# Performance work log

Measured on AMD Instinct MI355X. Metric: run time of the kernel, lower is better.

## Reference

```python
import jax, jax.numpy as jnp
import numpy as np

D_MODEL = 1024
NUM_HEADS = 16
HEAD_DIM = D_MODEL // NUM_HEADS


def setup_inputs() -> dict:
    key = jax.random.key(0)
    k1, k2, k3, k4, k5 = jax.random.split(key, 5)
    B, S = 2, 2048
    X = jax.random.normal(k1, (B, S, D_MODEL), dtype=jnp.float32)
    Wqkv = jax.random.normal(k2, (3 * D_MODEL, D_MODEL), dtype=jnp.float32) * 0.02
    bqkv = jax.random.normal(k3, (3 * D_MODEL,), dtype=jnp.float32) * 0.02
    Wo = jax.random.normal(k4, (D_MODEL, D_MODEL), dtype=jnp.float32) * 0.02
    bo = jax.random.normal(k5, (D_MODEL,), dtype=jnp.float32) * 0.02
    return {"X": X, "Wqkv": Wqkv, "bqkv": bqkv, "Wo": Wo, "bo": bo}


def reference(X, Wqkv, bqkv, Wo, bo):
    B, S, D = X.shape
    # fused QKV projection (torch Linear: x @ W.T + b)
    qkv = X @ Wqkv.T + bqkv                                  # [B, S, 3D]
    qkv = qkv.reshape(B, S, NUM_HEADS, 3 * HEAD_DIM)
    qkv = jnp.transpose(qkv, (0, 2, 1, 3))                   # [B, H, S, 3*hd]
    q, k, v = jnp.split(qkv, 3, axis=-1)                     # each [B, H, S, hd]
    # naive scaled dot-product attention (materializes full SxS scores)
    scale = 1.0 / jnp.sqrt(jnp.asarray(HEAD_DIM, dtype=X.dtype))
    scores = jnp.einsum("bhqd,bhkd->bhqk", q, k) * scale     # [B, H, S, S]
    attn = jax.nn.softmax(scores, axis=-1)
    values = jnp.einsum("bhqk,bhkd->bhqd", attn, v)          # [B, H, S, hd]
    values = jnp.transpose(values, (0, 2, 1, 3)).reshape(B, S, D)
    return values @ Wo.T + bo
```

## Files before the change

kernel.cpp:

```cpp
#include <hip/hip_runtime.h>

#define DM    1024
#define NH    16
#define HD    64
#define SEQ   2048
#define BATCH 2
#define NQKV  3072
#define MTOT  4096

using half2v = __attribute__((ext_vector_type(2))) _Float16;
using half4  = __attribute__((ext_vector_type(4))) _Float16;
using half8  = __attribute__((ext_vector_type(8))) _Float16;
using f32x4  = __attribute__((ext_vector_type(4))) float;

typedef const __attribute__((address_space(1))) unsigned int* gp_t;
typedef __attribute__((address_space(3))) unsigned int* lp_t;

__device__ __forceinline__ void gl2lds16(const void* g, void* l) {
    __builtin_amdgcn_global_load_lds((gp_t)g, (lp_t)l, 16, 0, 0);
}

__device__ __forceinline__ f32x4 fzero4() {
    f32x4 v; v[0] = 0.f; v[1] = 0.f; v[2] = 0.f; v[3] = 0.f; return v;
}

__device__ __forceinline__ int sw8(int row, int col) {
    return (row << 6) | ((((col >> 3) ^ row) & 7) << 3) | (col & 7);
}

#define CSCALE 0.18033688011112042f

__device__ __forceinline__ half2v expp2(float a, float b) {
    return __builtin_bit_cast(half2v, __builtin_amdgcn_cvt_pkrtz(
        __builtin_amdgcn_exp2f(a), __builtin_amdgcn_exp2f(b)));
}

#define ACQ(N) do {                                             \
    asm volatile("s_waitcnt vmcnt(" #N ")" ::: "memory");       \
    __builtin_amdgcn_sched_barrier(0);                          \
    __builtin_amdgcn_s_barrier();                               \
    __builtin_amdgcn_sched_barrier(0);                          \
} while (0)
#define REL() do {                                              \
    __builtin_amdgcn_sched_barrier(0);                          \
    asm volatile("s_waitcnt lgkmcnt(0)" ::: "memory");          \
    __builtin_amdgcn_s_barrier();                               \
    __builtin_amdgcn_sched_barrier(0);                          \
} while (0)

__global__ __launch_bounds__(256) void cvt_all(const float* __restrict__ X,
                                               const float* __restrict__ W1,
                                               const float* __restrict__ W2,
                                               const float* __restrict__ bqkv,
                                               float* __restrict__ bscaled,
                                               _Float16* __restrict__ out) {
    const int nX = MTOT * DM / 4, nW1 = NQKV * DM / 4, nW2 = DM * DM / 4;
    int i = blockIdx.x * 256 + threadIdx.x;
    if (i < NQKV) {
        const float b = bqkv[i];
        bscaled[i] = ((i % 192) < 64) ? b * CSCALE : b;
    }
    if (i >= nX + nW1 + nW2) return;
    float4 f;
    float sc = 1.0f;
    if (i < nX) {
        f = reinterpret_cast<const float4*>(X)[i];
    } else if (i < nX + nW1) {
        const int off = i - nX;
        f = reinterpret_cast<const float4*>(W1)[off];
        const int row = off >> 8;
        if ((row % 192) < 64) sc = CSCALE;
    } else {
        f = reinterpret_cast<const float4*>(W2)[i - nX - nW1];
    }
    half4 h;
    h[0] = (_Float16)(f.x * sc); h[1] = (_Float16)(f.y * sc);
    h[2] = (_Float16)(f.z * sc); h[3] = (_Float16)(f.w * sc);
    reinterpret_cast<half4*>(out)[i] = h;
}

template <bool OUT_F16>
__global__ __launch_bounds__(256) void gemm_nt(const _Float16* __restrict__ A,
                                               const _Float16* __restrict__ B,
                                               const float* __restrict__ bias,
                                               void* __restrict__ Cout,
                                               int M, int N, int K) {
    __shared__ _Float16 lA[128 * 64];
    __shared__ _Float16 lB[128 * 64];
    const int tid = threadIdx.x;
    const int m0 = blockIdx.y * 128, n0 = blockIdx.x * 128;
    const int wave = tid >> 6, lane = tid & 63, quad = lane >> 4, l15 = lane & 15;
    const int wm = (wave & 1) * 64, wn = (wave >> 1) * 64;

    f32x4 acc[4][4];
#pragma unroll
    for (int i = 0; i < 4; ++i)
#pragma unroll
        for (int j = 0; j < 4; ++j) acc[i][j] = fzero4();

    const int cperm = (((tid & 7) ^ (tid >> 3)) & 7) * 8;
    const _Float16* Ab = A + (long)(m0 + (tid >> 3)) * K + cperm;
    const _Float16* Bb = B + (long)(n0 + (tid >> 3)) * K + cperm;
    char* lAp = (char*)lA + tid * 16;
    char* lBp = (char*)lB + tid * 16;

    for (int kt = 0; kt < K; kt += 64) {
        __syncthreads();
#pragma unroll
        for (int j = 0; j < 4; ++j) {
            gl2lds16(Ab + (long)j * 32 * K + kt, lAp + j * 4096);
            gl2lds16(Bb + (long)j * 32 * K + kt, lBp + j * 4096);
        }
        __syncthreads();
#pragma unroll
        for (int ks = 0; ks < 2; ++ks) {
            half8 af[4], bfr[4];
#pragma unroll
            for (int t = 0; t < 4; ++t) {
                af[t]  = *(const half8*)(lA + sw8(wm + t * 16 + l15, ks * 32 + quad * 8));
                bfr[t] = *(const half8*)(lB + sw8(wn + t * 16 + l15, ks * 32 + quad * 8));
            }
#pragma unroll
            for (int mt = 0; mt < 4; ++mt)
#pragma unroll
                for (int nt = 0; nt < 4; ++nt)
                    acc[mt][nt] = __builtin_amdgcn_mfma_f32_16x16x32_f16(
                        af[mt], bfr[nt], acc[mt][nt], 0, 0, 0);
        }
    }

    float bs[4];
#pragma unroll
    for (int nt = 0; nt < 4; ++nt) bs[nt] = bias[n0 + wn + nt * 16 + l15];

#pragma unroll
    for (int mt = 0; mt < 4; ++mt) {
#pragma unroll
        for (int r = 0; r < 4; ++r) {
            const int m = m0 + wm + mt * 16 + quad * 4 + r;
#pragma unroll
            for (int nt = 0; nt < 4; ++nt) {
                const int n = n0 + wn + nt * 16 + l15;
                const float v = acc[mt][nt][r] + bs[nt];
                if constexpr (OUT_F16)
                    ((_Float16*)Cout)[(long)m * N + n] = (_Float16)v;
                else
                    ((float*)Cout)[(long)m * N + n] = v;
            }
        }
    }
}

template <bool OUT_F16>
__global__ __launch_bounds__(256) void gemm_nt_64(const _Float16* __restrict__ A,
                                                  const _Float16* __restrict__ B,
                                                  const float* __restrict__ bias,
                                                  void* __restrict__ Cout,
                                                  int M, int N, int K) {
    __shared__ _Float16 lA[64 * 64];
    __shared__ _Float16 lB[128 * 64];
    const int tid = threadIdx.x;
    const int m0 = blockIdx.y * 64, n0 = blockIdx.x * 128;
    const int wave = tid >> 6, lane = tid & 63, quad = lane >> 4, l15 = lane & 15;
    const int wm = (wave & 1) * 32, wn = (wave >> 1) * 64;

    f32x4 acc[2][4];
#pragma unroll
    for (int i = 0; i < 2; ++i)
#pragma unroll
        for (int j = 0; j < 4; ++j) acc[i][j] = fzero4();

    const int cperm = (((tid & 7) ^ (tid >> 3)) & 7) * 8;
    const _Float16* Ab = A + (long)(m0 + (tid >> 3)) * K + cperm;
    const _Float16* Bb = B + (long)(n0 + (tid >> 3)) * K + cperm;
    char* lAp = (char*)lA + tid * 16;
    char* lBp = (char*)lB + tid * 16;

    for (int kt = 0; kt < K; kt += 64) {
        __syncthreads();
#pragma unroll
        for (int j = 0; j < 2; ++j)
            gl2lds16(Ab + (long)j * 32 * K + kt, lAp + j * 4096);
#pragma unroll
        for (int j = 0; j < 4; ++j)
            gl2lds16(Bb + (long)j * 32 * K + kt, lBp + j * 4096);
        __syncthreads();
#pragma unroll
        for (int ks = 0; ks < 2; ++ks) {
            half8 af[2], bfr[4];
#pragma unroll
            for (int t = 0; t < 2; ++t)
                af[t] = *(const half8*)(lA + sw8(wm + t * 16 + l15, ks * 32 + quad * 8));
#pragma unroll
            for (int t = 0; t < 4; ++t)
                bfr[t] = *(const half8*)(lB + sw8(wn + t * 16 + l15, ks * 32 + quad * 8));
#pragma unroll
            for (int mt = 0; mt < 2; ++mt)
#pragma unroll
                for (int nt = 0; nt < 4; ++nt)
                    acc[mt][nt] = __builtin_amdgcn_mfma_f32_16x16x32_f16(
                        af[mt], bfr[nt], acc[mt][nt], 0, 0, 0);
        }
    }

    float bs[4];
#pragma unroll
    for (int nt = 0; nt < 4; ++nt) bs[nt] = bias[n0 + wn + nt * 16 + l15];

#pragma unroll
    for (int mt = 0; mt < 2; ++mt) {
#pragma unroll
        for (int r = 0; r < 4; ++r) {
            const int m = m0 + wm + mt * 16 + quad * 4 + r;
#pragma unroll
            for (int nt = 0; nt < 4; ++nt) {
                const int n = n0 + wn + nt * 16 + l15;
                const float v = acc[mt][nt][r] + bs[nt];
                if constexpr (OUT_F16)
                    ((_Float16*)Cout)[(long)m * N + n] = (_Float16)v;
                else
                    ((float*)Cout)[(long)m * N + n] = v;
            }
        }
    }
}

__global__ __launch_bounds__(256) void repack_v(const _Float16* __restrict__ qkvh,
                                                _Float16* __restrict__ vt) {
    const int b = blockIdx.z, h = blockIdx.y, s0 = blockIdx.x * 32;
    const int d = threadIdx.x & 63, si = threadIdx.x >> 6;
    const _Float16* src = qkvh + (long)(b * SEQ + s0) * NQKV + h * 192 + 128 + d;
    half8 v;
#pragma unroll
    for (int hi = 0; hi < 2; ++hi)
#pragma unroll
        for (int r = 0; r < 4; ++r)
            v[hi * 4 + r] = src[(long)(hi * 16 + si * 4 + r) * NQKV];
    *(half8*)(vt + (long)((b * NH + h) * HD + d) * SEQ + s0 + si * 8) = v;
}

__global__ __launch_bounds__(256) void attn_flash(const _Float16* __restrict__ qkv,
                                                  const _Float16* __restrict__ vt,
                                                  _Float16* __restrict__ aout) {
    __shared__ _Float16 lbuf[6][64 * 64];

    const int L = blockIdx.x + 16 * blockIdx.y + 256 * blockIdx.z;
    const int c = L & 7, j = L >> 3;
    const int pair = c * 4 + (j >> 4);
    const int b = pair >> 4, h = pair & 15;
    const int q0 = (j & 15) * 128;

    const int tid = threadIdx.x;
    const int wave = tid >> 6, lane = tid & 63, quad = lane >> 4, l15 = lane & 15;
    const int cperm8 = (((tid & 7) ^ (tid >> 3)) & 7) * 8;
    const int srow = tid >> 3;

    const _Float16* qsrc = qkv + (long)(b * SEQ + q0 + srow) * NQKV + h * 192 + cperm8;
#pragma unroll
    for (int jq = 0; jq < 4; ++jq)
        gl2lds16(qsrc + (long)jq * 32 * NQKV, (char*)lbuf + jq * 4096 + tid * 16);
    __syncthreads();

    half8 qf[2][2];
#pragma unroll
    for (int qt = 0; qt < 2; ++qt)
#pragma unroll
        for (int ks = 0; ks < 2; ++ks)
            qf[qt][ks] = *(const half8*)((const _Float16*)lbuf +
                             sw8(wave * 32 + qt * 16 + l15, ks * 32 + quad * 8));
    __syncthreads();

    f32x4 O[2][4];
#pragma unroll
    for (int qt = 0; qt < 2; ++qt)
#pragma unroll
        for (int dt = 0; dt < 4; ++dt) O[qt][dt] = fzero4();
    f32x4 lsum[2] = {fzero4(), fzero4()};

    half8 ones;
#pragma unroll
    for (int i = 0; i < 8; ++i) ones[i] = (_Float16)1.0f;

    const _Float16* ksrc = qkv + (long)(b * SEQ + srow) * NQKV + h * 192 + 64 + cperm8;
    const _Float16* vsrc = vt + (long)((b * NH + h) * HD + srow) * SEQ + cperm8;

#pragma unroll
    for (int jj = 0; jj < 2; ++jj) {
        gl2lds16(ksrc + (long)(jj * 32) * NQKV, (char*)lbuf[0] + jj * 4096 + tid * 16);
        gl2lds16(vsrc + (long)(jj * 32) * SEQ,  (char*)lbuf[3] + jj * 4096 + tid * 16);
    }
#pragma unroll
    for (int jj = 0; jj < 2; ++jj) {
        gl2lds16(ksrc + (long)(64 + jj * 32) * NQKV, (char*)lbuf[1] + jj * 4096 + tid * 16);
        gl2lds16(vsrc + (long)(jj * 32) * SEQ + 64,  (char*)lbuf[4] + jj * 4096 + tid * 16);
    }

    auto compute = [&](const _Float16* lK, const _Float16* lV) {
#pragma unroll
        for (int t = 0; t < 2; ++t) {
            f32x4 s[2][2];
            s[0][0] = fzero4(); s[0][1] = fzero4();
            s[1][0] = fzero4(); s[1][1] = fzero4();
#pragma unroll
            for (int tt = 0; tt < 2; ++tt)
#pragma unroll
                for (int ks = 0; ks < 2; ++ks) {
                    half8 kf = *(const half8*)(lK + sw8((2 * t + tt) * 16 + l15, ks * 32 + quad * 8));
                    s[0][tt] = __builtin_amdgcn_mfma_f32_16x16x32_f16(kf, qf[0][ks], s[0][tt], 0, 0, 0);
                    s[1][tt] = __builtin_amdgcn_mfma_f32_16x16x32_f16(kf, qf[1][ks], s[1][tt], 0, 0, 0);
                }
            half8 pf[2];
#pragma unroll
            for (int qt = 0; qt < 2; ++qt) {
                half2v p01 = expp2(s[qt][0][0], s[qt][0][1]);
                half2v p23 = expp2(s[qt][0][2], s[qt][0][3]);
                half2v p45 = expp2(s[qt][1][0], s[qt][1][1]);
                half2v p67 = expp2(s[qt][1][2], s[qt][1][3]);
                half4 lo = __builtin_shufflevector(p01, p23, 0, 1, 2, 3);
                half4 hi = __builtin_shufflevector(p45, p67, 0, 1, 2, 3);
                pf[qt] = __builtin_shufflevector(lo, hi, 0, 1, 2, 3, 4, 5, 6, 7);
                lsum[qt] = __builtin_amdgcn_mfma_f32_16x16x32_f16(pf[qt], ones, lsum[qt], 0, 0, 0);
            }
#pragma unroll
            for (int dt = 0; dt < 4; ++dt) {
                half8 vf = *(const half8*)(lV + sw8(dt * 16 + l15, t * 32 + quad * 8));
                O[0][dt] = __builtin_amdgcn_mfma_f32_16x16x32_f16(pf[0], vf, O[0][dt], 0, 0, 0);
                O[1][dt] = __builtin_amdgcn_mfma_f32_16x16x32_f16(pf[1], vf, O[1][dt], 0, 0, 0);
            }
        }
    };

    int cur = 0;
    for (int it = 0; it < 30; ++it) {
        int pre = cur + 2; if (pre >= 3) pre -= 3;
        const long s0n = (long)(it + 2) * 64;
#pragma unroll
        for (int jj = 0; jj < 2; ++jj) {
            gl2lds16(ksrc + (s0n + jj * 32) * NQKV,     (char*)lbuf[pre] + jj * 4096 + tid * 16);
            gl2lds16(vsrc + (long)(jj * 32) * SEQ + s0n, (char*)lbuf[3 + pre] + jj * 4096 + tid * 16);
        }
        ACQ(8);
        compute(lbuf[cur], lbuf[3 + cur]);
        REL();
        cur = (cur == 2) ? 0 : cur + 1;
    }
    ACQ(4);
    compute(lbuf[cur], lbuf[3 + cur]);
    REL();
    cur = (cur == 2) ? 0 : cur + 1;
    ACQ(0);
    compute(lbuf[cur], lbuf[3 + cur]);

#pragma unroll
    for (int qt = 0; qt < 2; ++qt) {
#pragma unroll
        for (int r = 0; r < 4; ++r) {
            const float lr = 1.0f / lsum[qt][r];
            const int row = b * SEQ + q0 + wave * 32 + qt * 16 + quad * 4 + r;
#pragma unroll
            for (int dt = 0; dt < 4; ++dt)
                aout[(long)row * DM + h * HD + dt * 16 + l15] =
                    (_Float16)(O[qt][dt][r] * lr);
        }
    }
}

extern "C" void kernel_launch(void* const* d_in, const int* in_sizes, int n_in,
                              void* d_out, int out_size, void* d_ws, size_t ws_size,
                              hipStream_t stream) {
    const float* X    = (const float*)d_in[0];
    const float* Wqkv = (const float*)d_in[1];
    const float* bqkv = (const float*)d_in[2];
    const float* Wo   = (const float*)d_in[3];
    const float* bo   = (const float*)d_in[4];

    char* ws = (char*)d_ws;
    _Float16* Xh   = (_Float16*)(ws);
    _Float16* Wqh  = (_Float16*)(ws + (size_t)8  * 1048576);
    _Float16* Woh  = (_Float16*)(ws + (size_t)14 * 1048576);
    _Float16* qkvh = (_Float16*)(ws + (size_t)16 * 1048576);
    _Float16* vth  = (_Float16*)(ws + (size_t)40 * 1048576);
    _Float16* atth = (_Float16*)(ws + (size_t)48 * 1048576);
    float* bscaled = (float*)(ws + (size_t)48 * 1048576);

    const int ncvt = (MTOT * DM + NQKV * DM + DM * DM) / 4;
    cvt_all<<<(ncvt + 255) / 256, 256, 0, stream>>>(X, Wqkv, Wo, bqkv, bscaled, Xh);

    gemm_nt<true><<<dim3(NQKV / 128, MTOT / 128), 256, 0, stream>>>(
        Xh, Wqh, bscaled, qkvh, MTOT, NQKV, DM);

    repack_v<<<dim3(SEQ / 32, NH, BATCH), 256, 0, stream>>>(qkvh, vth);

    attn_flash<<<dim3(SEQ / 128, NH, BATCH), 256, 0, stream>>>(qkvh, vth, atth);

    gemm_nt_64<false><<<dim3(DM / 128, MTOT / 64), 256, 0, stream>>>(
        atth, Woh, bo, d_out, MTOT, DM, DM);
}
```

Baseline: 196.1 us.

## Split attention KV range across two wave groups with LDS reduction

Doubles the attention block to 512 threads: two groups of four waves each process alternating 64-key tiles of a 128-key stage, using double-buffered 128-key stages. The partial O and row sums from the second group are reduced through LDS into the first group before normalization. This is meant to give more waves per block to hide latency and halve per-wave serial work. In exchange it costs more LDS, an extra reduction pass, and higher register pressure under the 512 launch bound.

```diff
diff --git a/kernel.cpp b/kernel.cpp
--- a/kernel.cpp
+++ b/kernel.cpp
@@ -239,10 +239,10 @@
     *(half8*)(vt + (long)((b * NH + h) * HD + d) * SEQ + s0 + si * 8) = v;
 }
 
-__global__ __launch_bounds__(256) void attn_flash(const _Float16* __restrict__ qkv,
+__global__ __launch_bounds__(512) void attn_flash(const _Float16* __restrict__ qkv,
                                                   const _Float16* __restrict__ vt,
                                                   _Float16* __restrict__ aout) {
-    __shared__ _Float16 lbuf[6][64 * 64];
+    __shared__ _Float16 lbuf[8][64 * 64];
 
     const int L = blockIdx.x + 16 * blockIdx.y + 256 * blockIdx.z;
     const int c = L & 7, j = L >> 3;
@@ -252,13 +252,14 @@
 
     const int tid = threadIdx.x;
     const int wave = tid >> 6, lane = tid & 63, quad = lane >> 4, l15 = lane & 15;
+    const int wq = wave & 3;
+    const int g  = wave >> 2;
     const int cperm8 = (((tid & 7) ^ (tid >> 3)) & 7) * 8;
     const int srow = tid >> 3;
 
     const _Float16* qsrc = qkv + (long)(b * SEQ + q0 + srow) * NQKV + h * 192 + cperm8;
-#pragma unroll
-    for (int jq = 0; jq < 4; ++jq)
-        gl2lds16(qsrc + (long)jq * 32 * NQKV, (char*)lbuf + jq * 4096 + tid * 16);
+    gl2lds16(qsrc,                   (char*)lbuf + tid * 16);
+    gl2lds16(qsrc + (long)64 * NQKV, (char*)lbuf + 8192 + tid * 16);
     __syncthreads();
 
     half8 qf[2][2];
@@ -267,7 +268,7 @@
 #pragma unroll
         for (int ks = 0; ks < 2; ++ks)
             qf[qt][ks] = *(const half8*)((const _Float16*)lbuf +
-                             sw8(wave * 32 + qt * 16 + l15, ks * 32 + quad * 8));
+                             sw8(wq * 32 + qt * 16 + l15, ks * 32 + quad * 8));
     __syncthreads();
 
     f32x4 O[2][4];
@@ -285,17 +286,15 @@
     const _Float16* vsrc = vt + (long)((b * NH + h) * HD + srow) * SEQ + cperm8;
 
 #pragma unroll
-    for (int jj = 0; jj < 2; ++jj) {
-        gl2lds16(ksrc + (long)(jj * 32) * NQKV, (char*)lbuf[0] + jj * 4096 + tid * 16);
-        gl2lds16(vsrc + (long)(jj * 32) * SEQ,  (char*)lbuf[3] + jj * 4096 + tid * 16);
-    }
-#pragma unroll
-    for (int jj = 0; jj < 2; ++jj) {
-        gl2lds16(ksrc + (long)(64 + jj * 32) * NQKV, (char*)lbuf[1] + jj * 4096 + tid * 16);
-        gl2lds16(vsrc + (long)(jj * 32) * SEQ + 64,  (char*)lbuf[4] + jj * 4096 + tid * 16);
-    }
-
-    auto compute = [&](const _Float16* lK, const _Float16* lV) {
+    for (int s = 0; s < 2; ++s) {
+        const long kb = (long)s * 128;
+        gl2lds16(ksrc + kb * NQKV,         (char*)lbuf[s * 4 + 0] + tid * 16);
+        gl2lds16(ksrc + (kb + 64) * NQKV,  (char*)lbuf[s * 4 + 1] + tid * 16);
+        gl2lds16(vsrc + kb,                (char*)lbuf[s * 4 + 2] + tid * 16);
+        gl2lds16(vsrc + kb + 64,           (char*)lbuf[s * 4 + 3] + tid * 16);
+    }
+
+    auto computeg = [&](const _Float16* lK, const _Float16* lV) {
 #pragma unroll
         for (int t = 0; t < 2; ++t) {
             f32x4 s[2][2];
@@ -330,37 +329,65 @@
         }
     };
 
-    int cur = 0;
-    for (int it = 0; it < 30; ++it) {
-        int pre = cur + 2; if (pre >= 3) pre -= 3;
-        const long s0n = (long)(it + 2) * 64;
-#pragma unroll
-        for (int jj = 0; jj < 2; ++jj) {
-            gl2lds16(ksrc + (s0n + jj * 32) * NQKV,     (char*)lbuf[pre] + jj * 4096 + tid * 16);
-            gl2lds16(vsrc + (long)(jj * 32) * SEQ + s0n, (char*)lbuf[3 + pre] + jj * 4096 + tid * 16);
-        }
-        ACQ(8);
-        compute(lbuf[cur], lbuf[3 + cur]);
+    ACQ(4);
+    computeg(lbuf[g], lbuf[2 + g]);
+    REL();
+    for (int it = 1; it <= 14; ++it) {
+        const int ns = ((it + 1) & 1) * 4;
+        const long kb = (long)(it + 1) * 128;
+        gl2lds16(ksrc + kb * NQKV,        (char*)lbuf[ns + 0] + tid * 16);
+        gl2lds16(ksrc + (kb + 64) * NQKV, (char*)lbuf[ns + 1] + tid * 16);
+        gl2lds16(vsrc + kb,               (char*)lbuf[ns + 2] + tid * 16);
+        gl2lds16(vsrc + kb + 64,          (char*)lbuf[ns + 3] + tid * 16);
+        const int cs = (it & 1) * 4;
+        ACQ(4);
+        computeg(lbuf[cs + g], lbuf[cs + 2 + g]);
         REL();
-        cur = (cur == 2) ? 0 : cur + 1;
-    }
-    ACQ(4);
-    compute(lbuf[cur], lbuf[3 + cur]);
-    REL();
-    cur = (cur == 2) ? 0 : cur + 1;
+    }
     ACQ(0);
-    compute(lbuf[cur], lbuf[3 + cur]);
-
-#pragma unroll
-    for (int qt = 0; qt < 2; ++qt) {
-#pragma unroll
-        for (int r = 0; r < 4; ++r) {
-            const float lr = 1.0f / lsum[qt][r];
-            const int row = b * SEQ + q0 + wave * 32 + qt * 16 + quad * 4 + r;
+    computeg(lbuf[4 + g], lbuf[6 + g]);
+    __syncthreads();
+
+    float* red = (float*)lbuf;
+    const int slot = (wq * 64 + lane) * 41;
+    if (wave >= 4) {
+        float* p = red + slot;
+#pragma unroll
+        for (int qt = 0; qt < 2; ++qt)
 #pragma unroll
             for (int dt = 0; dt < 4; ++dt)
-                aout[(long)row * DM + h * HD + dt * 16 + l15] =
-                    (_Float16)(O[qt][dt][r] * lr);
+#pragma unroll
+                for (int r = 0; r < 4; ++r) p[qt * 16 + dt * 4 + r] = O[qt][dt][r];
+#pragma unroll
+        for (int qt = 0; qt < 2; ++qt)
+#pragma unroll
+            for (int r = 0; r < 4; ++r) p[32 + qt * 4 + r] = lsum[qt][r];
+    }
+    __syncthreads();
+    if (wave < 4) {
+        const float* p = red + slot;
+#pragma unroll
+        for (int qt = 0; qt < 2; ++qt)
+#pragma unroll
+            for (int dt = 0; dt < 4; ++dt)
+#pragma unroll
+                for (int r = 0; r < 4; ++r) O[qt][dt][r] += p[qt * 16 + dt * 4 + r];
+#pragma unroll
+        for (int qt = 0; qt < 2; ++qt)
+#pragma unroll
+            for (int r = 0; r < 4; ++r) lsum[qt][r] += p[32 + qt * 4 + r];
+
+#pragma unroll
+        for (int qt = 0; qt < 2; ++qt) {
+#pragma unroll
+            for (int r = 0; r < 4; ++r) {
+                const float lr = 1.0f / lsum[qt][r];
+                const int row = b * SEQ + q0 + wq * 32 + qt * 16 + quad * 4 + r;
+#pragma unroll
+                for (int dt = 0; dt < 4; ++dt)
+                    aout[(long)row * DM + h * HD + dt * 16 + l15] =
+                        (_Float16)(O[qt][dt][r] * lr);
+            }
         }
     }
 }
@@ -391,7 +418,7 @@
 
     repack_v<<<dim3(SEQ / 32, NH, BATCH), 256, 0, stream>>>(qkvh, vth);
 
-    attn_flash<<<dim3(SEQ / 128, NH, BATCH), 256, 0, stream>>>(qkvh, vth, atth);
+    attn_flash<<<dim3(SEQ / 128, NH, BATCH), 512, 0, stream>>>(qkvh, vth, atth);
 
     gemm_nt_64<false><<<dim3(DM / 128, MTOT / 64), 256, 0, stream>>>(
         atth, Woh, bo, d_out, MTOT, DM, DM);
```

Result: faster. 179.6 us (-8.4%).
